# Kernel optimization log

Measured on AMD Instinct MI355X. Metric: run time of the kernel, lower is better.

## Reference

```python
import jax, jax.numpy as jnp
import numpy as np

B, N, DEG = 8, 8192, 16
E = B * N * DEG
K1 = 2458  # ceil(0.3*8192)
K2 = 738   # ceil(0.3*2458)
NUM_CLASSES = 10


def gat(x, src, dst, emask, W, a_s, a_d, bias):
    # PyG GATConv with add_self_loops=True, negative_slope=0.2, concat heads
    n = x.shape[0]
    H, F = a_s.shape
    xp = (x @ W).reshape(n, H, F)                      # [n,H,F]
    al_s = (xp * a_s).sum(-1)                          # [n,H]
    al_d = (xp * a_d).sum(-1)
    loops = jnp.arange(n, dtype=src.dtype)
    s2 = jnp.concatenate([src, loops])
    d2 = jnp.concatenate([dst, loops])
    m2 = jnp.concatenate([emask, jnp.ones(n, bool)])
    e = jax.nn.leaky_relu(al_s[s2] + al_d[d2], 0.2)    # [E+n,H]
    e = jnp.where(m2[:, None], e, -1e9)
    emax = jax.ops.segment_max(e, d2, num_segments=n)
    ex = jnp.where(m2[:, None], jnp.exp(e - emax[d2]), 0.0)
    den = jax.ops.segment_sum(ex, d2, num_segments=n)
    msg = ex[:, :, None] * xp[s2]                      # [E+n,H,F]
    out = jax.ops.segment_sum(msg, d2, num_segments=n) / den[:, :, None]
    return out.reshape(n, H * F) + bias


def inorm(x):
    # PyG InstanceNorm (affine=False): per-graph per-channel normalization
    xb = x.reshape(B, -1, x.shape[-1])
    mu = xb.mean(1, keepdims=True)
    var = ((xb - mu) ** 2).mean(1, keepdims=True)
    return ((xb - mu) / jnp.sqrt(var + 1e-5)).reshape(x.shape)


def topk_pool(x, src, dst, emask, p, k):
    # TopKPooling: score = tanh(x.p/|p|), keep top-k per graph, scale x by score
    n_tot = x.shape[0]
    n = n_tot // B
    score = jnp.tanh((x @ p) / jnp.linalg.norm(p))
    sv, si = jax.lax.top_k(score.reshape(B, n), k)     # [B,k]
    xg = jnp.take_along_axis(x.reshape(B, n, -1), si[:, :, None], axis=1)
    xnew = (xg * sv[:, :, None]).reshape(B * k, -1)
    perm = (si + (jnp.arange(B) * n)[:, None]).reshape(-1)
    newid = jnp.full(n_tot, -1, dtype=src.dtype).at[perm].set(
        jnp.arange(B * k, dtype=src.dtype))
    ns, nd = newid[src], newid[dst]
    m = emask & (ns >= 0) & (nd >= 0)
    return xnew, jnp.maximum(ns, 0), jnp.maximum(nd, 0), m


def setup_inputs() -> dict:
    key = jax.random.key(0)
    ks = jax.random.split(key, 32)
    pos = jax.random.normal(ks[0], (B * N, 3), jnp.float32)
    offs = jnp.repeat(jnp.arange(B, dtype=jnp.int32) * N, N * DEG)
    src = jax.random.randint(ks[1], (E,), 0, N, jnp.int32) + offs
    dst = jax.random.randint(ks[2], (E,), 0, N, jnp.int32) + offs

    def lin(k, fi, fo):
        return jax.random.normal(k, (fi, fo), jnp.float32) * (1.0 / np.sqrt(fi))

    d = dict(pos=pos, src=src, dst=dst)
    d['W1'] = lin(ks[3], 3, 32);   d['a_s1'] = jax.random.normal(ks[4], (2, 16)) * 0.2
    d['a_d1'] = jax.random.normal(ks[5], (2, 16)) * 0.2
    d['b1'] = jnp.zeros((32,));    d['p1'] = jax.random.normal(ks[6], (32,))
    d['W2'] = lin(ks[7], 32, 128); d['a_s2'] = jax.random.normal(ks[8], (2, 64)) * 0.2
    d['a_d2'] = jax.random.normal(ks[9], (2, 64)) * 0.2
    d['b2'] = jnp.zeros((128,));   d['p2'] = jax.random.normal(ks[10], (128,))
    d['W3'] = lin(ks[11], 128, 256); d['a_s3'] = jax.random.normal(ks[12], (1, 256)) * 0.1
    d['a_d3'] = jax.random.normal(ks[13], (1, 256)) * 0.1
    d['b3'] = jnp.zeros((256,))
    d['gw1'] = lin(ks[14], 256, 64);  d['gb1'] = jnp.zeros((64,))
    d['gw2'] = lin(ks[15], 64, 1);    d['gb2'] = jnp.zeros((1,))
    d['aw'] = lin(ks[16], 256, 256);  d['ab'] = jnp.zeros((256,))
    d['w1'] = lin(ks[17], 256, 512);  d['bb1'] = jnp.zeros((512,))
    d['w2'] = lin(ks[18], 512, 128);  d['bb2'] = jnp.zeros((128,))
    d['w3'] = lin(ks[19], 128, NUM_CLASSES); d['bb3'] = jnp.zeros((NUM_CLASSES,))
    return d


def reference(pos, src, dst, W1, a_s1, a_d1, b1, p1, W2, a_s2, a_d2, b2, p2,
              W3, a_s3, a_d3, b3, gw1, gb1, gw2, gb2, aw, ab,
              w1, bb1, w2, bb2, w3, bb3):
    emask = jnp.ones(src.shape[0], bool)
    x = gat(pos, src, dst, emask, W1, a_s1, a_d1, b1)
    x = jax.nn.elu(inorm(x))
    x, src, dst, emask = topk_pool(x, src, dst, emask, p1, K1)
    x = gat(x, src, dst, emask, W2, a_s2, a_d2, b2)
    x = jax.nn.elu(inorm(x))
    x, src, dst, emask = topk_pool(x, src, dst, emask, p2, K2)
    x = gat(x, src, dst, emask, W3, a_s3, a_d3, b3)
    x = jax.nn.elu(inorm(x))
    # GlobalAttention: gate_nn = Linear(256,64)+ELU+Linear(64,1); nn = Linear+ELU
    gate = jax.nn.elu(x @ gw1 + gb1) @ gw2 + gb2       # [M,1]
    h = jax.nn.elu(x @ aw + ab)                        # [M,256]
    a = jax.nn.softmax(gate.reshape(B, K2, 1), axis=1)
    g = (a * h.reshape(B, K2, 256)).sum(1)             # [B,256]
    z = jax.nn.elu(g @ w1 + bb1)   # dropout inactive in eval
    z = jax.nn.elu(z @ w2 + bb2)
    z = z @ w3 + bb3
    return jax.nn.log_softmax(z, axis=1)
```

## Files before the change

### kernel.cpp

```cpp
#include <hip/hip_runtime.h>
#include <cstdint>
#include <cstddef>

#define DI __device__ __forceinline__

namespace pk {

constexpr int NB1 = 65536;
constexpr int NE  = 1048576;
constexpr int BG  = 8;
constexpr int NPG1 = 8192;
constexpr int EPG1 = NE/BG;
constexpr int KP1 = 2458;
constexpr int KP2 = 738;
constexpr int NN2 = BG*KP1;
constexpr int NN3 = BG*KP2;
constexpr int REG2 = 16384;
constexpr int REG3 = 4096;
constexpr int CAP2 = BG*REG2;
constexpr int CAP3 = BG*REG3;

DI float lrelu(float x){ return x > 0.f ? x : 0.2f*x; }
DI float eluf(float x){ return x > 0.f ? x : expf(x) - 1.f; }

DI int swz_block(){
  int nb = gridDim.x, b = blockIdx.x;
  if((nb & 7) == 0) return (b & 7)*(nb >> 3) + (b >> 3);
  return b;
}

__global__ __launch_bounds__(256) void k_xp1(
    const float* __restrict__ pos, const float* __restrict__ W,
    const float* __restrict__ as_, const float* __restrict__ ad_,
    float* __restrict__ xp, float* __restrict__ als, float* __restrict__ ald){
  int i = blockIdx.x*256 + threadIdx.x;
  if(i >= NB1) return;
  float p0=pos[3*i], p1=pos[3*i+1], p2=pos[3*i+2];
  float row[32];
#pragma unroll
  for(int c=0;c<32;c++) row[c] = p0*W[c] + p1*W[32+c] + p2*W[64+c];
  float s0=0.f,d0=0.f,s1=0.f,d1=0.f;
#pragma unroll
  for(int f=0;f<16;f++){
    s0 += row[f]*as_[f];        d0 += row[f]*ad_[f];
    s1 += row[16+f]*as_[16+f];  d1 += row[16+f]*ad_[16+f];
  }
  float4* o = reinterpret_cast<float4*>(xp + (size_t)i*32);
#pragma unroll
  for(int q=0;q<8;q++) o[q] = make_float4(row[4*q],row[4*q+1],row[4*q+2],row[4*q+3]);
  als[2*i]=s0; als[2*i+1]=s1; ald[2*i]=d0; ald[2*i+1]=d1;
}

__global__ __launch_bounds__(1024) void k_tile_count(
    const int* __restrict__ de, int* __restrict__ cnt){
  __shared__ int h[256];
  int tid = threadIdx.x;
  int g = blockIdx.x & 7, t = blockIdx.x >> 3;
  int lo = g*NPG1 + t*256;
  if(tid < 256) h[tid] = 0;
  __syncthreads();
  const int4* de4 = (const int4*)(de + g*EPG1);
  for(int it=0; it<4; it++){
    int4 buf[8];
#pragma unroll
    for(int j=0;j<8;j++) buf[j] = de4[(it*8+j)*1024 + tid];
#pragma unroll
    for(int j=0;j<8;j++){
      int4 b = buf[j];
      int d0=b.x-lo, d1=b.y-lo, d2=b.z-lo, d3=b.w-lo;
      if((unsigned)d0<256u) atomicAdd(&h[d0],1);
      if((unsigned)d1<256u) atomicAdd(&h[d1],1);
      if((unsigned)d2<256u) atomicAdd(&h[d2],1);
      if((unsigned)d3<256u) atomicAdd(&h[d3],1);
    }
  }
  __syncthreads();
  if(tid < 256) cnt[lo + tid] = h[tid];
}

__global__ __launch_bounds__(1024) void k_tile_scatter(
    const int* __restrict__ se, const int* __restrict__ de,
    const int* __restrict__ rowptr, int* __restrict__ eo){
  __shared__ int cur[256];
  int tid = threadIdx.x;
  int g = blockIdx.x & 7, t = blockIdx.x >> 3;
  int lo = g*NPG1 + t*256;
  if(tid < 256) cur[tid] = rowptr[lo + tid];
  __syncthreads();
  const int4* de4 = (const int4*)(de + g*EPG1);
  const int4* se4 = (const int4*)(se + g*EPG1);
  for(int it=0; it<4; it++){
    int4 bd[8], bs[8];
#pragma unroll
    for(int j=0;j<8;j++){
      int idx = (it*8+j)*1024 + tid;
      bd[j] = de4[idx]; bs[j] = se4[idx];
    }
#pragma unroll
    for(int j=0;j<8;j++){
      int4 d = bd[j], s = bs[j];
      int d0=d.x-lo; if((unsigned)d0<256u){ int p=atomicAdd(&cur[d0],1); eo[p]=s.x; }
      int d1=d.y-lo; if((unsigned)d1<256u){ int p=atomicAdd(&cur[d1],1); eo[p]=s.y; }
      int d2=d.z-lo; if((unsigned)d2<256u){ int p=atomicAdd(&cur[d2],1); eo[p]=s.z; }
      int d3=d.w-lo; if((unsigned)d3<256u){ int p=atomicAdd(&cur[d3],1); eo[p]=s.w; }
    }
  }
}

__global__ __launch_bounds__(256) void k_scatter_r(
    const int* __restrict__ se, const int* __restrict__ de,
    const int* __restrict__ gcnt, int reg,
    int* __restrict__ cursor, int* __restrict__ eo){
  int i = swz_block()*256 + threadIdx.x;
  int g = i / reg, loc = i % reg;
  if(loc < gcnt[g]){
    int p = atomicAdd(&cursor[de[i]], 1);
    eo[p] = se[i];
  }
}

__global__ __launch_bounds__(256) void k_edge_compact(
    const int* __restrict__ se, const int* __restrict__ de,
    const int* __restrict__ gcnt_in, int fixed_in, int bpg, int reg_in,
    const int* __restrict__ newid, int* __restrict__ gcnt_out,
    int* __restrict__ ons, int* __restrict__ ond, int reg_out,
    int* __restrict__ cnt){
  __shared__ int s_a[4096];
  __shared__ int s_b[4096];
  __shared__ int run, tbase;
  int tid = threadIdx.x;
  if(tid == 0) run = 0;
  __syncthreads();
  int blk = swz_block();
  int g = blk / bpg, t = blk % bpg;
  int mg = gcnt_in ? gcnt_in[g] : fixed_in;
  if(mg > reg_in) mg = reg_in;
  int base_l = t*4096;
  if(base_l < mg){
    const int* deb = de + (size_t)g*reg_in + base_l;
    const int* seb = se + (size_t)g*reg_in + base_l;
    const int4* de4 = (const int4*)deb;
    const int4* se4 = (const int4*)seb;
    int4 BD[4], BS[4];
#pragma unroll
    for(int j=0;j<4;j++){ BD[j]=de4[j*256+tid]; BS[j]=se4[j*256+tid]; }
#pragma unroll
    for(int j=0;j<4;j++){
      int eb = base_l + (j*256+tid)*4;
      int dd[4]={BD[j].x,BD[j].y,BD[j].z,BD[j].w};
      int ss[4]={BS[j].x,BS[j].y,BS[j].z,BS[j].w};
#pragma unroll
      for(int q=0;q<4;q++){
        if(eb+q < mg){
          int a = newid[ss[q]], b = newid[dd[q]];
          if(a>=0 && b>=0){
            int p = atomicAdd(&run, 1);
            s_a[p]=a; s_b[p]=b;
            atomicAdd(&cnt[b], 1);
          }
        }
      }
    }
  }
  __syncthreads();
  int ns = run;
  if(tid==0) tbase = ns ? atomicAdd(&gcnt_out[g], ns) : 0;
  __syncthreads();
  int tb = tbase;
  for(int j=tid; j<ns; j+=256){
    int s2 = tb + j;
    if(s2 < reg_out){ ons[(size_t)g*reg_out+s2]=s_a[j]; ond[(size_t)g*reg_out+s2]=s_b[j]; }
  }
}

__global__ __launch_bounds__(1024) void k_scan_g(
    const int* __restrict__ cnt, int R, int estride,
    int* __restrict__ rowptr, int* __restrict__ cursor){
  __shared__ int wsum[16];
  int g = blockIdx.x;
  int tid = threadIdx.x, lane = tid & 63, w = tid >> 6;
  int PER = (R + 1023) >> 10;
  int base = g*R;
  int i0 = tid*PER;
  int v[8]; int s = 0;
  for(int j=0;j<PER;j++){ int i=i0+j; int x=(i<R)?cnt[base+i]:0; v[j]=s; s+=x; }
  int inc = s;
  for(int o=1;o<64;o<<=1){ int t=__shfl_up(inc,o,64); if(lane>=o) inc+=t; }
  if(lane==63) wsum[w]=inc;
  __syncthreads();
  int wb=0;
  for(int k=0;k<w;k++) wb+=wsum[k];
  int tb = g*estride + wb + inc - s;
  for(int j=0;j<PER;j++){
    int i=i0+j;
    if(i<R){
      int e=tb+v[j];
      rowptr[base+i]=e;
      if(cursor) cursor[base+i]=e;
    }
  }
}

template<int H,int F,int ECAP>
__global__ __launch_bounds__(256) void k_gat_fused(
    const float* __restrict__ xp, const float* __restrict__ als,
    const float* __restrict__ ald, const int* __restrict__ rowptr,
    const int* __restrict__ cnt, const int* __restrict__ esrc,
    const float* __restrict__ bias, float* __restrict__ out,
    float* __restrict__ accum, int RPG, int n){
  constexpr int C = H*F, C4 = C/4, NPB = 256/C4;
  __shared__ int rst[NPB];
  __shared__ int ecum[NPB+1];
  __shared__ float aldv[NPB*H];
  __shared__ float wselfs[NPB*H];
  __shared__ float dens[NPB*H];
  __shared__ float wexps[ECAP*H];
  __shared__ float psum[4][C], psq[4][C];
  int tid = threadIdx.x;
  int node0 = swz_block()*NPB;
  if(tid < NPB){
    int node = node0 + tid;
    rst[tid] = (node < n) ? rowptr[node] : 0;
  }
  if(tid < 64){
    int d = (tid < NPB && node0+tid < n) ? cnt[node0+tid] : 0;
    int inc = d;
    for(int o=1;o<64;o<<=1){ int t2=__shfl_up(inc,o,64); if(tid>=o) inc+=t2; }
    if(tid < NPB) ecum[tid] = inc - d;
    if(tid == NPB-1) ecum[NPB] = inc;
  }
  if(tid < NPB*H){
    int node = node0 + tid/H, h = tid%H;
    float dv = 0.f, sw = 0.f;
    if(node < n){ dv = ald[node*H+h]; sw = expf(lrelu(als[node*H+h] + dv)); }
    aldv[tid]=dv; wselfs[tid]=sw; dens[tid]=sw;
  }
  __syncthreads();
  int totE = ecum[NPB];
  for(int s=tid; s<totE; s+=256){
    int lo=0, hi=NPB;
    while(hi-lo > 1){ int mid=(lo+hi)>>1; if(ecum[mid] <= s) lo=mid; else hi=mid; }
    int k = rst[lo] + (s - ecum[lo]);
    int srcn = esrc[k];
    if(H == 2){
      float2 a = ((const float2*)als)[srcn];
      float e0 = expf(lrelu(a.x + aldv[lo*2]));
      float e1 = expf(lrelu(a.y + aldv[lo*2+1]));
      if(s < ECAP){ wexps[s*2]=e0; wexps[s*2+1]=e1; }
      atomicAdd(&dens[lo*2], e0);
      atomicAdd(&dens[lo*2+1], e1);
    } else {
      float e0 = expf(lrelu(als[srcn] + aldv[lo]));
      if(s < ECAP) wexps[s]=e0;
      atomicAdd(&dens[lo], e0);
    }
  }
  __syncthreads();
  int nl = tid / C4, p = tid % C4;
  int node = node0 + nl;
  int hh = (4*p)/F;
  const float4* xp4 = (const float4*)xp;
  float4 r = make_float4(0.f,0.f,0.f,0.f);
  bool valid = node < n;
  if(valid){
    float4 xs = xp4[(size_t)node*C4 + p];
    float sw = wselfs[nl*H+hh];
    float ax=sw*xs.x, ay=sw*xs.y, az=sw*xs.z, aw_=sw*xs.w;
    int r0 = rst[nl], e0o = ecum[nl], deg = ecum[nl+1]-e0o;
    float dvh = aldv[nl*H+hh];
#pragma unroll 4
    for(int j=0;j<deg;j++){
      int s = e0o + j;
      int srcn = esrc[r0+j];
      float w = (s < ECAP) ? wexps[s*H+hh]
                           : expf(lrelu(als[srcn*H+hh] + dvh));
      float4 v = xp4[(size_t)srcn*C4 + p];
      ax+=w*v.x; ay+=w*v.y; az+=w*v.z; aw_+=w*v.w;
    }
    float inv = 1.f / dens[nl*H+hh];
    float4 bv = ((const float4*)bias)[p];
    r.x=ax*inv+bv.x; r.y=ay*inv+bv.y; r.z=az*inv+bv.z; r.w=aw_*inv+bv.w;
    ((float4*)out)[(size_t)node*C4 + p] = r;
  }
  int g0 = node0 / RPG;
  bool straddle = ((node0 + NPB - 1) / RPG) != g0;
  if(straddle){
    if(valid){
      int g = node / RPG;
      atomicAdd(&accum[(g*C+4*p+0)*2], r.x); atomicAdd(&accum[(g*C+4*p+0)*2+1], r.x*r.x);
      atomicAdd(&accum[(g*C+4*p+1)*2], r.y); atomicAdd(&accum[(g*C+4*p+1)*2+1], r.y*r.y);
      atomicAdd(&accum[(g*C+4*p+2)*2], r.z); atomicAdd(&accum[(g*C+4*p+2)*2+1], r.z*r.z);
      atomicAdd(&accum[(g*C+4*p+3)*2], r.w); atomicAdd(&accum[(g*C+4*p+3)*2+1], r.w*r.w);
    }
  } else {
    float sx=r.x, sy=r.y, sz=r.z, sw2=r.w;
    float qx=r.x*r.x, qy=r.y*r.y, qz=r.z*r.z, qw=r.w*r.w;
#pragma unroll
    for(int off=C4; off<64; off<<=1){
      sx += __shfl_down(sx, off, 64); sy += __shfl_down(sy, off, 64);
      sz += __shfl_down(sz, off, 64); sw2 += __shfl_down(sw2, off, 64);
      qx += __shfl_down(qx, off, 64); qy += __shfl_down(qy, off, 64);
      qz += __shfl_down(qz, off, 64); qw += __shfl_down(qw, off, 64);
    }
    int lane = tid & 63, w = tid >> 6;
    if(lane < C4){
      psum[w][4*lane+0]=sx; psum[w][4*lane+1]=sy;
      psum[w][4*lane+2]=sz; psum[w][4*lane+3]=sw2;
      psq[w][4*lane+0]=qx;  psq[w][4*lane+1]=qy;
      psq[w][4*lane+2]=qz;  psq[w][4*lane+3]=qw;
    }
    __syncthreads();
    if(tid < C){
      float ts = psum[0][tid]+psum[1][tid]+psum[2][tid]+psum[3][tid];
      float tq = psq[0][tid]+psq[1][tid]+psq[2][tid]+psq[3][tid];
      atomicAdd(&accum[(g0*C+tid)*2],   ts);
      atomicAdd(&accum[(g0*C+tid)*2+1], tq);
    }
  }
}

template<int K,int CO,int NPG,int H>
__global__ __launch_bounds__(256) void k_gemm_al(
    const float* __restrict__ X, const int* __restrict__ oldid,
    const float* __restrict__ scale, const float* __restrict__ W,
    float* __restrict__ Y, const float* __restrict__ a_s,
    const float* __restrict__ a_d, float* __restrict__ als,
    float* __restrict__ ald, int n){
  constexpr int SUB = 256/CO;
  constexpr int NB = SUB*NPG;
  __shared__ float xs[NB][K];
  __shared__ float ps[4][NPG], pd[4][NPG];
  int tid = threadIdx.x;
  int c = tid % CO, sg = tid / CO;
  int n0 = blockIdx.x * NB;
  for(int idx=tid; idx<NB*K; idx+=256){
    int r = idx / K, k = idx % K;
    int row = n0 + r;
    float v = 0.f;
    if(row < n){
      int orow = oldid[row];
      v = X[(size_t)orow*K + k] * scale[row];
    }
    xs[r][k] = v;
  }
  __syncthreads();
  float acc[NPG];
#pragma unroll
  for(int q=0;q<NPG;q++) acc[q]=0.f;
  for(int k=0;k<K;k++){
    float wv = W[(size_t)k*CO + c];
#pragma unroll
    for(int q=0;q<NPG;q++) acc[q] += xs[sg*NPG+q][k]*wv;
  }
  float asc = a_s[c], adc = a_d[c];
  float vs[NPG], vd[NPG];
#pragma unroll
  for(int q=0;q<NPG;q++){
    int row = n0 + sg*NPG + q;
    if(row < n) Y[(size_t)row*CO + c] = acc[q];
    vs[q] = acc[q]*asc; vd[q] = acc[q]*adc;
  }
#pragma unroll
  for(int o=32;o>0;o>>=1){
#pragma unroll
    for(int q=0;q<NPG;q++){
      vs[q] += __shfl_down(vs[q], o, 64);
      vd[q] += __shfl_down(vd[q], o, 64);
    }
  }
  int lane = tid & 63, w = tid >> 6;
  if(H == 2){
    if(lane == 0){
      int sg_ = w >> 1, h = w & 1;
#pragma unroll
      for(int q=0;q<NPG;q++){
        int row = n0 + sg_*NPG + q;
        if(row < n){ als[row*2+h] = vs[q]; ald[row*2+h] = vd[q]; }
      }
    }
  } else {
    if(lane == 0){
#pragma unroll
      for(int q=0;q<NPG;q++){ ps[w][q]=vs[q]; pd[w][q]=vd[q]; }
    }
    __syncthreads();
    if(tid < NPG){
      float s=0.f, d=0.f;
      for(int ww=0;ww<4;ww++){ s+=ps[ww][tid]; d+=pd[ww][tid]; }
      int row = n0 + tid;
      if(row < n){ als[row]=s; ald[row]=d; }
    }
  }
}

DI float inorm_of(const float* accum, int gc, float R, float x){
  float s = accum[gc*2], sq = accum[gc*2+1];
  float mu = s / R;
  float var = fmaxf(sq/R - mu*mu, 0.f);
  return eluf((x-mu)*rsqrtf(var+1e-5f));
}

template<int C>
__global__ __launch_bounds__(256) void k_inorm_score(
    float* __restrict__ x, const float* __restrict__ accum,
    const float* __restrict__ p, int R, int total,
    float* __restrict__ score, unsigned* __restrict__ u){
  __shared__ float rvp[256], rpp[256];
  int tid = threadIdx.x;
  int i = blockIdx.x*256 + tid;
  int c = tid & (C-1);
  bool act = i < total;
  float v = 0.f, pv = 0.f;
  if(act){
    int g = i / (R*C);
    v = inorm_of(accum, g*C+c, (float)R, x[i]);
    x[i] = v;
    pv = p[c];
  }
  rvp[tid] = v*pv; rpp[tid] = pv*pv;
  __syncthreads();
#pragma unroll
  for(int s2=C/2; s2>0; s2>>=1){
    if(c < s2){ rvp[tid]+=rvp[tid+s2]; rpp[tid]+=rpp[tid+s2]; }
    __syncthreads();
  }
  if(act && c==0){
    float sv = tanhf(rvp[tid]*rsqrtf(rpp[tid]));
    int row = i / C;
    score[row] = sv;
    unsigned bts = __float_as_uint(sv);
    u[row] = (bts & 0x80000000u) ? ~bts : (bts | 0x80000000u);
  }
}

__global__ __launch_bounds__(1024) void k_topk(
    const unsigned* __restrict__ u, const float* __restrict__ score,
    int R, int Ksel, int* __restrict__ newid, int* __restrict__ oldid,
    float* __restrict__ scale){
  __shared__ int hist[2048];
  __shared__ int seg[32];
  __shared__ int sh_b, sh_k;
  __shared__ int wsA[16], wsB[16];
  __shared__ int carr0, carr1;
  int g = blockIdx.x, tid = threadIdx.x, lane = tid&63, w = tid>>6;
  const unsigned* ug = u + (size_t)g*R;
  unsigned prefix = 0;
  int K = Ksel;
  for(int lev=0; lev<3; lev++){
    int shf = (lev==0)?21:((lev==1)?10:0);
    int nb  = (lev==2)?1024:2048;
    for(int i=tid;i<2048;i+=1024) hist[i]=0;
    __syncthreads();
    for(int i=tid;i<R;i+=1024){
      unsigned v = ug[i];
      bool ok = (lev==0) || (lev==1 && (v>>21)==prefix) || (lev==2 && (v>>10)==prefix);
      if(ok) atomicAdd(&hist[(v>>shf)&(nb-1)], 1);
    }
    __syncthreads();
    int W = nb/32;
    if(tid<32){ int s=0; int lo=nb-W*(tid+1); for(int b=lo;b<lo+W;b++) s+=hist[b]; seg[tid]=s; }
    __syncthreads();
    if(tid==0){
      int kk=K, sgi=0;
      while(seg[sgi]<kk){ kk-=seg[sgi]; sgi++; }
      int b = nb-1-W*sgi;
      while(hist[b]<kk){ kk-=hist[b]; b--; }
      sh_b=b; sh_k=kk;
    }
    __syncthreads();
    int b = sh_b; K = sh_k;
    if(lev==0) prefix = (unsigned)b;
    else if(lev==1) prefix = (prefix<<11) | (unsigned)b;
    else prefix = (prefix<<10) | (unsigned)b;
    __syncthreads();
  }
  unsigned thr = prefix;
  int need = K;
  if(tid==0){ carr0=0; carr1=0; }
  __syncthreads();
  for(int bb=0; bb<R; bb+=1024){
    int i = bb + tid; bool in = i < R;
    unsigned uv = in ? ug[i] : 0u;
    int eq = (in && uv==thr) ? 1:0;
    int gt = (in && uv>thr) ? 1:0;
    int inc = eq;
    for(int o=1;o<64;o<<=1){ int t=__shfl_up(inc,o,64); if(lane>=o) inc+=t; }
    if(lane==63) wsA[w]=inc;
    __syncthreads();
    int wb=0; for(int k=0;k<w;k++) wb+=wsA[k];
    int eq_excl = carr0 + wb + inc - eq;
    int take = (gt || (eq && eq_excl<need)) ? 1 : 0;
    int inc2 = take;
    for(int o=1;o<64;o<<=1){ int t=__shfl_up(inc2,o,64); if(lane>=o) inc2+=t; }
    if(lane==63) wsB[w]=inc2;
    __syncthreads();
    int wb2=0; for(int k=0;k<w;k++) wb2+=wsB[k];
    int pos = carr1 + wb2 + inc2 - take;
    if(take){
      int nr = g*Ksel + pos;
      newid[(size_t)g*R+i] = nr;
      oldid[nr] = g*R+i;
      scale[nr] = score[(size_t)g*R+i];
    }
    __syncthreads();
    if(tid==1023){ carr0 += wb + inc; carr1 += wb2 + inc2; }
    __syncthreads();
  }
}

__global__ __launch_bounds__(256) void k_gate_fused(
    const float* __restrict__ X, const float* __restrict__ accum,
    const float* __restrict__ gw1, const float* __restrict__ gb1,
    const float* __restrict__ gw2, const float* __restrict__ gb2,
    float* __restrict__ gatev, int n){
  __shared__ float xs[4][256];
  int tid = threadIdx.x;
  int n0 = blockIdx.x*4;
  for(int idx=tid; idx<1024; idx+=256){
    int r = idx >> 8, k = idx & 255;
    int row = n0 + r;
    float v = 0.f;
    if(row < n){
      int g = row / KP2;
      v = inorm_of(accum, g*256+k, (float)KP2, X[(size_t)row*256 + k]);
    }
    xs[r][k] = v;
  }
  __syncthreads();
  int sg = tid >> 6, c = tid & 63;
  float a = 0.f;
#pragma unroll 8
  for(int k=0;k<256;k++) a = fmaf(xs[sg][k], gw1[k*64+c], a);
  a = eluf(a + gb1[c]);
  float v = a * gw2[c];
#pragma unroll
  for(int o=32;o>0;o>>=1) v += __shfl_down(v, o, 64);
  if(c==0){
    int row = n0 + sg;
    if(row < n) gatev[row] = v + gb2[0];
  }
}

__global__ __launch_bounds__(256) void k_attn_gemm(
    const float* __restrict__ X, const float* __restrict__ accum,
    const float* __restrict__ W, const float* __restrict__ bias,
    const float* __restrict__ gatev, float* __restrict__ gvec){
  __shared__ float xs[4][256];
  __shared__ float red[256];
  int tid = threadIdx.x;
  int t = blockIdx.x, g = blockIdx.y;
  int r0 = t*4;
  float mx = -1e30f;
  for(int r=tid;r<KP2;r+=256) mx = fmaxf(mx, gatev[g*KP2+r]);
  red[tid]=mx; __syncthreads();
  for(int s=128;s>0;s>>=1){ if(tid<s) red[tid]=fmaxf(red[tid],red[tid+s]); __syncthreads(); }
  mx = red[0]; __syncthreads();
  float sm=0.f;
  for(int r=tid;r<KP2;r+=256) sm += expf(gatev[g*KP2+r]-mx);
  red[tid]=sm; __syncthreads();
  for(int s=128;s>0;s>>=1){ if(tid<s) red[tid]+=red[tid+s]; __syncthreads(); }
  float inv = 1.f/red[0];
  __syncthreads();
  for(int idx=tid; idx<1024; idx+=256){
    int r = idx >> 8, k = idx & 255;
    int lr = r0 + r;
    float v = 0.f;
    if(lr < KP2){
      int row = g*KP2 + lr;
      v = inorm_of(accum, g*256+k, (float)KP2, X[(size_t)row*256 + k]);
    }
    xs[r][k] = v;
  }
  __syncthreads();
  int c = tid;
  float acc[4];
#pragma unroll
  for(int q=0;q<4;q++) acc[q]=0.f;
  for(int k=0;k<256;k++){
    float wv = W[(size_t)k*256 + c];
#pragma unroll
    for(int q=0;q<4;q++) acc[q] += xs[q][k]*wv;
  }
  float bv = bias[c];
  float tot = 0.f;
#pragma unroll
  for(int q=0;q<4;q++){
    int lr = r0 + q;
    if(lr < KP2){
      float h = eluf(acc[q] + bv);
      tot += expf(gatev[g*KP2+lr]-mx) * h;
    }
  }
  atomicAdd(&gvec[g*256+c], tot*inv);
}

template<int K,int CO,int ACT>
__global__ __launch_bounds__(256) void k_mlp_t(
    const float* __restrict__ X, const float* __restrict__ W,
    const float* __restrict__ b, float* __restrict__ Y, int n){
  int i = blockIdx.x*256+threadIdx.x;
  if(i>=n*CO) return;
  int r=i/CO, c=i%CO;
  const float* xr = X + (size_t)r*K;
  float a=0.f;
#pragma unroll 16
  for(int k=0;k<K;k++) a = fmaf(xr[k], W[(size_t)k*CO+c], a);
  a += b[c];
  if(ACT) a = eluf(a);
  Y[i]=a;
}

__global__ __launch_bounds__(64) void k_head(
    const float* __restrict__ z2, const float* __restrict__ w3,
    const float* __restrict__ b3, float* __restrict__ out){
  __shared__ float zc[10]; __shared__ float mred, sred;
  int g=blockIdx.x, tid=threadIdx.x;
  if(tid<10){
    float a=0.f;
#pragma unroll 16
    for(int k=0;k<128;k++) a += z2[g*128+k]*w3[k*10+tid];
    zc[tid]=a+b3[tid];
  }
  __syncthreads();
  if(tid==0){
    float m=zc[0];
    for(int k=1;k<10;k++) m=fmaxf(m,zc[k]);
    float s=0.f;
    for(int k=0;k<10;k++) s+=expf(zc[k]-m);
    mred=m; sred=logf(s);
  }
  __syncthreads();
  if(tid<10) out[g*10+tid]=zc[tid]-mred-sred;
}

}

extern "C" void kernel_launch(void* const* d_in, const int* in_sizes, int n_in,
                              void* d_out, int out_size, void* d_ws, size_t ws_size,
                              hipStream_t stream){
  using namespace pk;
  (void)in_sizes; (void)n_in; (void)out_size;
  const float* pos = (const float*)d_in[0];
  const int*   src = (const int*)d_in[1];
  const int*   dst = (const int*)d_in[2];
  const float* W1  = (const float*)d_in[3];
  const float* as1 = (const float*)d_in[4];
  const float* ad1 = (const float*)d_in[5];
  const float* b1  = (const float*)d_in[6];
  const float* p1  = (const float*)d_in[7];
  const float* W2  = (const float*)d_in[8];
  const float* as2 = (const float*)d_in[9];
  const float* ad2 = (const float*)d_in[10];
  const float* b2  = (const float*)d_in[11];
  const float* p2  = (const float*)d_in[12];
  const float* W3  = (const float*)d_in[13];
  const float* as3 = (const float*)d_in[14];
  const float* ad3 = (const float*)d_in[15];
  const float* b3  = (const float*)d_in[16];
  const float* gw1 = (const float*)d_in[17];
  const float* gb1 = (const float*)d_in[18];
  const float* gw2 = (const float*)d_in[19];
  const float* gb2 = (const float*)d_in[20];
  const float* aw  = (const float*)d_in[21];
  const float* ab  = (const float*)d_in[22];
  const float* w1  = (const float*)d_in[23];
  const float* bb1 = (const float*)d_in[24];
  const float* w2  = (const float*)d_in[25];
  const float* bb2 = (const float*)d_in[26];
  const float* w3  = (const float*)d_in[27];
  const float* bb3 = (const float*)d_in[28];
  float* out = (float*)d_out;

  char* base = (char*)d_ws; size_t off = 0;
  auto alloc = [&](size_t nbytes)->char*{
    char* p = base + off; off = (off + nbytes + 255) & ~(size_t)255; return p;
  };
  int*   cnt2  = (int*)alloc((size_t)NN2*4);
  int*   cnt3  = (int*)alloc((size_t)NN3*4);
  int*   ecnt2 = (int*)alloc((size_t)BG*4);
  int*   ecnt3 = (int*)alloc((size_t)BG*4);
  float* acc1  = (float*)alloc((size_t)BG*32*2*4);
  float* acc2  = (float*)alloc((size_t)BG*128*2*4);
  float* acc3  = (float*)alloc((size_t)BG*256*2*4);
  float* gvec  = (float*)alloc((size_t)BG*256*4);
  size_t zend = off;
  int*   newid1 = (int*)alloc((size_t)NB1*4);
  int*   newid2 = (int*)alloc((size_t)NN2*4);
  size_t fstart = (size_t)((char*)newid1 - base);
  size_t fend = off;
  int*      cnt1   = (int*)alloc((size_t)NB1*4);
  float*    xp1    = (float*)alloc((size_t)NB1*32*4);
  float*    als1   = (float*)alloc((size_t)NB1*2*4);
  float*    ald1   = (float*)alloc((size_t)NB1*2*4);
  int*      rowptr1= (int*)alloc((size_t)NB1*4);
  int*      esrc1  = (int*)alloc((size_t)NE*4);
  float*    out1   = (float*)alloc((size_t)NB1*32*4);
  float*    score1 = (float*)alloc((size_t)NB1*4);
  unsigned* u1     = (unsigned*)alloc((size_t)NB1*4);
  int*      oldid1 = (int*)alloc((size_t)NN2*4);
  float*    scale1 = (float*)alloc((size_t)NN2*4);
  int*      ns2    = (int*)alloc((size_t)CAP2*4);
  int*      nd2    = (int*)alloc((size_t)CAP2*4);
  int*      rowptr2= (int*)alloc((size_t)NN2*4);
  int*      cursor2= (int*)alloc((size_t)NN2*4);
  int*      esrc2  = (int*)alloc((size_t)CAP2*4);
  float*    xp2    = (float*)alloc((size_t)NN2*128*4);
  float*    als2   = (float*)alloc((size_t)NN2*2*4);
  float*    ald2   = (float*)alloc((size_t)NN2*2*4);
  float*    out2   = (float*)alloc((size_t)NN2*128*4);
  float*    score2 = (float*)alloc((size_t)NN2*4);
  unsigned* u2     = (unsigned*)alloc((size_t)NN2*4);
  int*      oldid2 = (int*)alloc((size_t)NN3*4);
  float*    scale2 = (float*)alloc((size_t)NN3*4);
  int*      ns3    = (int*)alloc((size_t)CAP3*4);
  int*      nd3    = (int*)alloc((size_t)CAP3*4);
  int*      rowptr3= (int*)alloc((size_t)NN3*4);
  int*      cursor3= (int*)alloc((size_t)NN3*4);
  int*      esrc3  = (int*)alloc((size_t)CAP3*4);
  float*    xp3    = (float*)alloc((size_t)NN3*256*4);
  float*    als3   = (float*)alloc((size_t)NN3*4);
  float*    ald3   = (float*)alloc((size_t)NN3*4);
  float*    out3   = (float*)alloc((size_t)NN3*256*4);
  float*    gatev  = (float*)alloc((size_t)NN3*4);
  float*    z1     = (float*)alloc((size_t)BG*512*4);
  float*    z2     = (float*)alloc((size_t)BG*128*4);
  if(off > ws_size) return;

  auto cdiv = [](int a, int b){ return (a+b-1)/b; };

  hipMemsetAsync(base, 0, zend, stream);
  hipMemsetAsync(base + fstart, 0xFF, fend - fstart, stream);

  k_xp1<<<cdiv(NB1,256),256,0,stream>>>(pos,W1,as1,ad1,xp1,als1,ald1);
  k_tile_count<<<256,1024,0,stream>>>(dst,cnt1);
  k_scan_g<<<BG,1024,0,stream>>>(cnt1,NPG1,EPG1,rowptr1,nullptr);
  k_tile_scatter<<<256,1024,0,stream>>>(src,dst,rowptr1,esrc1);
  k_gat_fused<2,16,768><<<NB1/32,256,0,stream>>>(xp1,als1,ald1,rowptr1,cnt1,esrc1,b1,out1,acc1,NPG1,NB1);
  k_inorm_score<32><<<cdiv(NB1*32,256),256,0,stream>>>(out1,acc1,p1,8192,NB1*32,score1,u1);
  k_topk<<<BG,1024,0,stream>>>(u1,score1,8192,KP1,newid1,oldid1,scale1);
  k_edge_compact<<<BG*32,256,0,stream>>>(src,dst,nullptr,EPG1,32,EPG1,newid1,ecnt2,ns2,nd2,REG2,cnt2);
  k_scan_g<<<BG,1024,0,stream>>>(cnt2,KP1,REG2,rowptr2,cursor2);
  k_scatter_r<<<CAP2/256,256,0,stream>>>(ns2,nd2,ecnt2,REG2,cursor2,esrc2);
  k_gemm_al<32,128,4,2><<<cdiv(NN2,8),256,0,stream>>>(out1,oldid1,scale1,W2,xp2,as2,ad2,als2,ald2,NN2);
  k_gat_fused<2,64,256><<<NN2/8,256,0,stream>>>(xp2,als2,ald2,rowptr2,cnt2,esrc2,b2,out2,acc2,KP1,NN2);
  k_inorm_score<128><<<cdiv(NN2*128,256),256,0,stream>>>(out2,acc2,p2,KP1,NN2*128,score2,u2);
  k_topk<<<BG,1024,0,stream>>>(u2,score2,KP1,KP2,newid2,oldid2,scale2);
  k_edge_compact<<<BG*4,256,0,stream>>>(ns2,nd2,ecnt2,0,4,REG2,newid2,ecnt3,ns3,nd3,REG3,cnt3);
  k_scan_g<<<BG,1024,0,stream>>>(cnt3,KP2,REG3,rowptr3,cursor3);
  k_scatter_r<<<CAP3/256,256,0,stream>>>(ns3,nd3,ecnt3,REG3,cursor3,esrc3);
  k_gemm_al<128,256,4,1><<<cdiv(NN3,4),256,0,stream>>>(out2,oldid2,scale2,W3,xp3,as3,ad3,als3,ald3,NN3);
  k_gat_fused<1,256,128><<<NN3/4,256,0,stream>>>(xp3,als3,ald3,rowptr3,cnt3,esrc3,b3,out3,acc3,KP2,NN3);
  k_gate_fused<<<cdiv(NN3,4),256,0,stream>>>(out3,acc3,gw1,gb1,gw2,gb2,gatev,NN3);
  k_attn_gemm<<<dim3(cdiv(KP2,4),BG),256,0,stream>>>(out3,acc3,aw,ab,gatev,gvec);
  k_mlp_t<256,512,1><<<cdiv(BG*512,256),256,0,stream>>>(gvec,w1,bb1,z1,BG);
  k_mlp_t<512,128,1><<<cdiv(BG*128,256),256,0,stream>>>(z1,w2,bb2,z2,BG);
  k_head<<<BG,64,0,stream>>>(z2,w3,bb3,out);
}
```

Measured before the change: 458.5 us.

## Drop shared-memory edge-weight precompute in GAT; batch neighbor gathers per thread

The fused GAT kernel no longer precomputes edge attention weights and denominators in shared memory with a block-wide edge loop, binary search and shared atomics. Each thread now recomputes the exp weights for its own head and builds the denominator itself. Neighbor indices, logits and features are gathered in batches of EB to expose memory-level parallelism. This removes two barriers and the shared atomics, at the cost of redundant exp work across the threads sharing a head and of padded gathers in the last batch.

```diff
diff --git a/kernel.cpp b/kernel.cpp
--- a/kernel.cpp
+++ b/kernel.cpp
@@ -201,83 +201,51 @@
   }
 }
 
-template<int H,int F,int ECAP>
+template<int H,int F,int EB>
 __global__ __launch_bounds__(256) void k_gat_fused(
     const float* __restrict__ xp, const float* __restrict__ als,
     const float* __restrict__ ald, const int* __restrict__ rowptr,
     const int* __restrict__ cnt, const int* __restrict__ esrc,
     const float* __restrict__ bias, float* __restrict__ out,
     float* __restrict__ accum, int RPG, int n){
-  constexpr int C = H*F, C4 = C/4, NPB = 256/C4;
-  __shared__ int rst[NPB];
-  __shared__ int ecum[NPB+1];
-  __shared__ float aldv[NPB*H];
-  __shared__ float wselfs[NPB*H];
-  __shared__ float dens[NPB*H];
-  __shared__ float wexps[ECAP*H];
+  constexpr int C = H*F, C4 = C/4;
+  constexpr int NPB = 256/C4;
   __shared__ float psum[4][C], psq[4][C];
   int tid = threadIdx.x;
+  int nl = tid / C4, p = tid % C4;
   int node0 = swz_block()*NPB;
-  if(tid < NPB){
-    int node = node0 + tid;
-    rst[tid] = (node < n) ? rowptr[node] : 0;
-  }
-  if(tid < 64){
-    int d = (tid < NPB && node0+tid < n) ? cnt[node0+tid] : 0;
-    int inc = d;
-    for(int o=1;o<64;o<<=1){ int t2=__shfl_up(inc,o,64); if(tid>=o) inc+=t2; }
-    if(tid < NPB) ecum[tid] = inc - d;
-    if(tid == NPB-1) ecum[NPB] = inc;
-  }
-  if(tid < NPB*H){
-    int node = node0 + tid/H, h = tid%H;
-    float dv = 0.f, sw = 0.f;
-    if(node < n){ dv = ald[node*H+h]; sw = expf(lrelu(als[node*H+h] + dv)); }
-    aldv[tid]=dv; wselfs[tid]=sw; dens[tid]=sw;
-  }
-  __syncthreads();
-  int totE = ecum[NPB];
-  for(int s=tid; s<totE; s+=256){
-    int lo=0, hi=NPB;
-    while(hi-lo > 1){ int mid=(lo+hi)>>1; if(ecum[mid] <= s) lo=mid; else hi=mid; }
-    int k = rst[lo] + (s - ecum[lo]);
-    int srcn = esrc[k];
-    if(H == 2){
-      float2 a = ((const float2*)als)[srcn];
-      float e0 = expf(lrelu(a.x + aldv[lo*2]));
-      float e1 = expf(lrelu(a.y + aldv[lo*2+1]));
-      if(s < ECAP){ wexps[s*2]=e0; wexps[s*2+1]=e1; }
-      atomicAdd(&dens[lo*2], e0);
-      atomicAdd(&dens[lo*2+1], e1);
-    } else {
-      float e0 = expf(lrelu(als[srcn] + aldv[lo]));
-      if(s < ECAP) wexps[s]=e0;
-      atomicAdd(&dens[lo], e0);
-    }
-  }
-  __syncthreads();
-  int nl = tid / C4, p = tid % C4;
   int node = node0 + nl;
   int hh = (4*p)/F;
   const float4* xp4 = (const float4*)xp;
   float4 r = make_float4(0.f,0.f,0.f,0.f);
   bool valid = node < n;
   if(valid){
+    float dvh = ald[node*H+hh];
+    float sw  = expf(lrelu(als[node*H+hh] + dvh));
     float4 xs = xp4[(size_t)node*C4 + p];
-    float sw = wselfs[nl*H+hh];
+    float den = sw;
     float ax=sw*xs.x, ay=sw*xs.y, az=sw*xs.z, aw_=sw*xs.w;
-    int r0 = rst[nl], e0o = ecum[nl], deg = ecum[nl+1]-e0o;
-    float dvh = aldv[nl*H+hh];
-#pragma unroll 4
-    for(int j=0;j<deg;j++){
-      int s = e0o + j;
-      int srcn = esrc[r0+j];
-      float w = (s < ECAP) ? wexps[s*H+hh]
-                           : expf(lrelu(als[srcn*H+hh] + dvh));
-      float4 v = xp4[(size_t)srcn*C4 + p];
-      ax+=w*v.x; ay+=w*v.y; az+=w*v.z; aw_+=w*v.w;
-    }
-    float inv = 1.f / dens[nl*H+hh];
+    int r0  = rowptr[node];
+    int deg = cnt[node];
+    for(int j=0; j<deg; j+=EB){
+      int idx[EB]; float wv[EB]; float4 v[EB];
+#pragma unroll
+      for(int q=0;q<EB;q++)
+        idx[q] = (j+q < deg) ? esrc[r0+j+q] : node;
+#pragma unroll
+      for(int q=0;q<EB;q++)
+        wv[q] = als[idx[q]*H+hh];
+#pragma unroll
+      for(int q=0;q<EB;q++)
+        v[q] = xp4[(size_t)idx[q]*C4 + p];
+#pragma unroll
+      for(int q=0;q<EB;q++){
+        float w = (j+q < deg) ? expf(lrelu(wv[q] + dvh)) : 0.f;
+        den += w;
+        ax += w*v[q].x; ay += w*v[q].y; az += w*v[q].z; aw_ += w*v[q].w;
+      }
+    }
+    float inv = 1.f / den;
     float4 bv = ((const float4*)bias)[p];
     r.x=ax*inv+bv.x; r.y=ay*inv+bv.y; r.z=az*inv+bv.z; r.w=aw_*inv+bv.w;
     ((float4*)out)[(size_t)node*C4 + p] = r;
@@ -735,21 +703,21 @@
   k_tile_count<<<256,1024,0,stream>>>(dst,cnt1);
   k_scan_g<<<BG,1024,0,stream>>>(cnt1,NPG1,EPG1,rowptr1,nullptr);
   k_tile_scatter<<<256,1024,0,stream>>>(src,dst,rowptr1,esrc1);
-  k_gat_fused<2,16,768><<<NB1/32,256,0,stream>>>(xp1,als1,ald1,rowptr1,cnt1,esrc1,b1,out1,acc1,NPG1,NB1);
+  k_gat_fused<2,16,8><<<NB1/32,256,0,stream>>>(xp1,als1,ald1,rowptr1,cnt1,esrc1,b1,out1,acc1,NPG1,NB1);
   k_inorm_score<32><<<cdiv(NB1*32,256),256,0,stream>>>(out1,acc1,p1,8192,NB1*32,score1,u1);
   k_topk<<<BG,1024,0,stream>>>(u1,score1,8192,KP1,newid1,oldid1,scale1);
   k_edge_compact<<<BG*32,256,0,stream>>>(src,dst,nullptr,EPG1,32,EPG1,newid1,ecnt2,ns2,nd2,REG2,cnt2);
   k_scan_g<<<BG,1024,0,stream>>>(cnt2,KP1,REG2,rowptr2,cursor2);
   k_scatter_r<<<CAP2/256,256,0,stream>>>(ns2,nd2,ecnt2,REG2,cursor2,esrc2);
   k_gemm_al<32,128,4,2><<<cdiv(NN2,8),256,0,stream>>>(out1,oldid1,scale1,W2,xp2,as2,ad2,als2,ald2,NN2);
-  k_gat_fused<2,64,256><<<NN2/8,256,0,stream>>>(xp2,als2,ald2,rowptr2,cnt2,esrc2,b2,out2,acc2,KP1,NN2);
+  k_gat_fused<2,64,8><<<NN2/8,256,0,stream>>>(xp2,als2,ald2,rowptr2,cnt2,esrc2,b2,out2,acc2,KP1,NN2);
   k_inorm_score<128><<<cdiv(NN2*128,256),256,0,stream>>>(out2,acc2,p2,KP1,NN2*128,score2,u2);
   k_topk<<<BG,1024,0,stream>>>(u2,score2,KP1,KP2,newid2,oldid2,scale2);
   k_edge_compact<<<BG*4,256,0,stream>>>(ns2,nd2,ecnt2,0,4,REG2,newid2,ecnt3,ns3,nd3,REG3,cnt3);
   k_scan_g<<<BG,1024,0,stream>>>(cnt3,KP2,REG3,rowptr3,cursor3);
   k_scatter_r<<<CAP3/256,256,0,stream>>>(ns3,nd3,ecnt3,REG3,cursor3,esrc3);
   k_gemm_al<128,256,4,1><<<cdiv(NN3,4),256,0,stream>>>(out2,oldid2,scale2,W3,xp3,as3,ad3,als3,ald3,NN3);
-  k_gat_fused<1,256,128><<<NN3/4,256,0,stream>>>(xp3,als3,ald3,rowptr3,cnt3,esrc3,b3,out3,acc3,KP2,NN3);
+  k_gat_fused<1,256,4><<<NN3/4,256,0,stream>>>(xp3,als3,ald3,rowptr3,cnt3,esrc3,b3,out3,acc3,KP2,NN3);
   k_gate_fused<<<cdiv(NN3,4),256,0,stream>>>(out3,acc3,gw1,gb1,gw2,gb2,gatev,NN3);
   k_attn_gemm<<<dim3(cdiv(KP2,4),BG),256,0,stream>>>(out3,acc3,aw,ab,gatev,gvec);
   k_mlp_t<256,512,1><<<cdiv(BG*512,256),256,0,stream>>>(gvec,w1,bb1,z1,BG);
```

Result: faster. 447.8 us (-2.3%).
